# Kernel optimization log

Hardware: AMD Instinct MI355X
Metric: run time of the kernel (lower is better)

The kernel has to match this reference:

```python
import jax, jax.numpy as jnp
import numpy as np

N_NODES = 50000
NUM_HEAD = 2
NEG_SLOPE_ATT = 0.2
NEG_SLOPE_ACT = 0.3


def _glorot(key, shape):
    fan = shape[-1] + (shape[-2] if len(shape) > 1 else shape[-1])
    lim = jnp.sqrt(6.0 / fan)
    return jax.random.uniform(key, shape, jnp.float32, -lim, lim)


def gat_conv(h, src, dst, W, att, bias):
    # h: (N, in_dim); W: (out_dim, in_dim) torch Linear layout; att: (1, H, 2k)
    N = h.shape[0]
    H = att.shape[1]
    k = att.shape[2] // 2
    x = (h @ W.T).reshape(N, H, k)
    x_i = x[dst]  # target features (E, H, k)
    x_j = x[src]  # source features (E, H, k)
    # alpha = sum(cat([x_i, x_j]) * att) without materializing the concat
    alpha = jnp.einsum('ehk,hk->eh', x_i, att[0, :, :k]) + jnp.einsum('ehk,hk->eh', x_j, att[0, :, k:])
    alpha = jax.nn.leaky_relu(alpha, NEG_SLOPE_ATT)
    # segment softmax grouped by edge_index[0] (src), as in the original code
    m = jax.ops.segment_max(alpha, src, num_segments=N)
    e = jnp.exp(alpha - m[src])
    s = jax.ops.segment_sum(e, src, num_segments=N)
    alpha = e / (s[src] + 1e-16)
    msg = x_j * alpha[:, :, None]
    out = jax.ops.segment_sum(msg, dst, num_segments=N)  # aggregate to targets
    out = out.reshape(N, H * k) + bias
    return jax.nn.relu(out)


def _forward(x, src, dst, node_index, params):
    (W1, att1, b1, W2, att2, b2, W3, att3, b3, W_out, b_out) = params
    h = gat_conv(x, src, dst, W1, att1, b1)
    h = jax.nn.leaky_relu(h, NEG_SLOPE_ACT)
    h = gat_conv(h, src, dst, W2, att2, b2)
    h = jax.nn.leaky_relu(h, NEG_SLOPE_ACT)
    h = gat_conv(h, src, dst, W3, att3, b3)
    x_embed = jax.nn.leaky_relu(h, NEG_SLOPE_ACT)
    output = x_embed @ W_out.T + b_out
    node_output = output[node_index]
    ypred = jnp.argmax(output, axis=1)
    y_nodepred = ypred[node_index]
    return x_embed, node_output, ypred, y_nodepred


def setup_inputs() -> dict:
    key = jax.random.key(0)
    ks = jax.random.split(key, 16)
    N, E, D = N_NODES, 800000, 128
    H, k = NUM_HEAD, 128 // NUM_HEAD
    inp = {
        'x': jax.random.normal(ks[0], (N, D), jnp.float32),
        'edge_index': jax.random.randint(ks[1], (2, E), 0, N, jnp.int64),
        'node_label': jax.random.normal(ks[2], (1000, 1, 3), jnp.float32),
        'node_index': jax.random.randint(ks[3], (1000,), 0, N, jnp.int64),
        'W1': _glorot(ks[4], (D, D)),
        'att1': _glorot(ks[5], (1, H, 2 * k)),
        'b1': jnp.zeros((D,), jnp.float32),
        'W2': _glorot(ks[6], (D, D)),
        'att2': _glorot(ks[7], (1, H, 2 * k)),
        'b2': jnp.zeros((D,), jnp.float32),
        'W3': _glorot(ks[8], (D, D)),
        'att3': _glorot(ks[9], (1, H, 2 * k)),
        'b3': jnp.zeros((D,), jnp.float32),
        'W_out': _glorot(ks[10], (3, D)),
        'b_out': jnp.zeros((3,), jnp.float32),
    }
    return inp


def reference(x, edge_index, node_label, node_index, W1, att1, b1, W2, att2, b2, W3, att3, b3, W_out, b_out):
    N = x.shape[0]
    loop = jnp.arange(N, dtype=edge_index.dtype)
    src = jnp.concatenate([edge_index[0], loop])  # add_self_loops
    dst = jnp.concatenate([edge_index[1], loop])
    params = (W1, att1, b1, W2, att2, b2, W3, att3, b3, W_out, b_out)
    return _forward(x, src, dst, node_index, params)
```

## Files before the change

### kernel.cpp

```cpp
#include <hip/hip_runtime.h>
#include <math.h>


#define EPB 8192

__global__ __launch_bounds__(256) void gemm128(const float* __restrict__ A,
                                               const float* __restrict__ Wm,
                                               const float* __restrict__ att,
                                               float* __restrict__ C,
                                               float4* __restrict__ ni4,
                                               float2* __restrict__ ad2v, int N) {
    __shared__ float As[64][68];
    __shared__ float Wt[64][132];
    const int tx = threadIdx.x;
    const int row0 = blockIdx.x * 64;
    const int cid = tx & 31;
    const int rid = tx >> 5;
    float acc[8][4] = {};
    const float4* A4 = (const float4*)A;
    const float4* W4 = (const float4*)Wm;

    for (int kt = 0; kt < 2; ++kt) {
        for (int i = tx; i < 1024; i += 256) {
            int r = i >> 4, q = i & 15;
            int row = row0 + r;
            float4 v = (row < N) ? A4[(size_t)row * 32 + kt * 16 + q]
                                 : make_float4(0.f, 0.f, 0.f, 0.f);
            As[r][q * 4 + 0] = v.x; As[r][q * 4 + 1] = v.y;
            As[r][q * 4 + 2] = v.z; As[r][q * 4 + 3] = v.w;
        }
        for (int i = tx; i < 2048; i += 256) {
            int c = i >> 4, q = i & 15;
            float4 v = W4[(size_t)c * 32 + kt * 16 + q];
            Wt[q * 4 + 0][c] = v.x; Wt[q * 4 + 1][c] = v.y;
            Wt[q * 4 + 2][c] = v.z; Wt[q * 4 + 3][c] = v.w;
        }
        __syncthreads();
        for (int k = 0; k < 64; k += 4) {
            float4 a[8];
            #pragma unroll
            for (int i = 0; i < 8; ++i) a[i] = *(const float4*)&As[rid * 8 + i][k];
            #pragma unroll
            for (int kk = 0; kk < 4; ++kk) {
                float4 w = *(const float4*)&Wt[k + kk][cid * 4];
                #pragma unroll
                for (int i = 0; i < 8; ++i) {
                    float av = (kk == 0) ? a[i].x : (kk == 1) ? a[i].y : (kk == 2) ? a[i].z : a[i].w;
                    acc[i][0] += av * w.x; acc[i][1] += av * w.y;
                    acc[i][2] += av * w.z; acc[i][3] += av * w.w;
                }
            }
        }
        __syncthreads();
    }
    #pragma unroll
    for (int i = 0; i < 8; ++i) {
        int row = row0 + rid * 8 + i;
        if (row < N)
            ((float4*)C)[(size_t)row * 32 + cid] =
                make_float4(acc[i][0], acc[i][1], acc[i][2], acc[i][3]);
    }
    const int hh = cid >> 4;
    const int c0 = (cid & 15) * 4;
    float ad0 = att[hh * 128 + c0 + 0], ad1 = att[hh * 128 + c0 + 1];
    float ad2c = att[hh * 128 + c0 + 2], ad3 = att[hh * 128 + c0 + 3];
    float as0 = att[hh * 128 + 64 + c0 + 0], as1 = att[hh * 128 + 64 + c0 + 1];
    float as2 = att[hh * 128 + 64 + c0 + 2], as3 = att[hh * 128 + 64 + c0 + 3];
    float pd[8], ps[8];
    #pragma unroll
    for (int i = 0; i < 8; ++i) {
        pd[i] = acc[i][0] * ad0 + acc[i][1] * ad1 + acc[i][2] * ad2c + acc[i][3] * ad3;
        ps[i] = acc[i][0] * as0 + acc[i][1] * as1 + acc[i][2] * as2 + acc[i][3] * as3;
    }
    #pragma unroll
    for (int m = 1; m < 16; m <<= 1) {
        #pragma unroll
        for (int i = 0; i < 8; ++i) {
            pd[i] += __shfl_xor(pd[i], m);
            ps[i] += __shfl_xor(ps[i], m);
        }
    }
    const int ll = tx & 63;
    const int grp = ll & 32;
    #pragma unroll
    for (int i = 0; i < 8; ++i) {
        float d0 = __shfl(pd[i], grp + 0);
        float d1 = __shfl(pd[i], grp + 16);
        float s0 = __shfl(ps[i], grp + 0);
        float s1 = __shfl(ps[i], grp + 16);
        if ((ll & 31) == 0) {
            int row = row0 + rid * 8 + i;
            if (row < N) {
                ad2v[row] = make_float2(d0, d1);
                ni4[row] = make_float4(s0, s1, 0.f, 0.f);
            }
        }
    }
}

__global__ __launch_bounds__(256) void init_deg(unsigned int* __restrict__ dd,
                                                unsigned int* __restrict__ ds, int N) {
    int n = blockIdx.x * 256 + threadIdx.x;
    if (n < N) { dd[n] = 1u; ds[n] = 1u; }
}

__global__ __launch_bounds__(256) void hist_both(const int* __restrict__ ei, int E,
                                                 unsigned int* __restrict__ dd,
                                                 unsigned int* __restrict__ ds) {
    int e = blockIdx.x * 256 + threadIdx.x;
    if (e < E) {
        atomicAdd(&ds[ei[e]], 1u);
        atomicAdd(&dd[ei[E + e]], 1u);
    }
}

__global__ __launch_bounds__(256) void scan_p1(const unsigned int* __restrict__ deg,
                                               unsigned int* __restrict__ off,
                                               unsigned int* __restrict__ bsum, int N) {
    __shared__ unsigned int sh[256];
    int t = threadIdx.x;
    int base = blockIdx.x * 1024 + t * 4;
    unsigned int v0 = 0, v1 = 0, v2 = 0, v3 = 0;
    if (base + 3 < N) {
        uint4 q = *(const uint4*)&deg[base];
        v0 = q.x; v1 = q.y; v2 = q.z; v3 = q.w;
    } else {
        if (base + 0 < N) v0 = deg[base + 0];
        if (base + 1 < N) v1 = deg[base + 1];
        if (base + 2 < N) v2 = deg[base + 2];
        if (base + 3 < N) v3 = deg[base + 3];
    }
    sh[t] = v0 + v1 + v2 + v3;
    __syncthreads();
    #pragma unroll
    for (int d = 1; d < 256; d <<= 1) {
        unsigned int u = (t >= d) ? sh[t - d] : 0u;
        __syncthreads();
        sh[t] += u;
        __syncthreads();
    }
    unsigned int ex = (t == 0) ? 0u : sh[t - 1];
    if (base + 3 < N) {
        *(uint4*)&off[base] = make_uint4(ex, ex + v0, ex + v0 + v1, ex + v0 + v1 + v2);
    } else {
        if (base + 0 < N) off[base + 0] = ex;
        if (base + 1 < N) off[base + 1] = ex + v0;
        if (base + 2 < N) off[base + 2] = ex + v0 + v1;
        if (base + 3 < N) off[base + 3] = ex + v0 + v1 + v2;
    }
    if (t == 255) bsum[blockIdx.x] = sh[255];
}

__global__ __launch_bounds__(1024) void scan_p2(unsigned int* __restrict__ bsum, int NB) {
    __shared__ unsigned int sh[1024];
    int t = threadIdx.x;
    sh[t] = (t < NB) ? bsum[t] : 0u;
    __syncthreads();
    #pragma unroll
    for (int d = 1; d < 1024; d <<= 1) {
        unsigned int u = (t >= d) ? sh[t - d] : 0u;
        __syncthreads();
        sh[t] += u;
        __syncthreads();
    }
    if (t < NB) bsum[t] = (t == 0) ? 0u : sh[t - 1];
}

__global__ __launch_bounds__(256) void scan_p3(unsigned int* __restrict__ off,
                                               const unsigned int* __restrict__ bsum,
                                               int N, unsigned int total) {
    int i = blockIdx.x * 256 + threadIdx.x;
    if (i < N) off[i] += bsum[i >> 10];
    if (i == N) off[N] = total;
}

__global__ __launch_bounds__(256) void init_cur(const unsigned int* __restrict__ off_d,
                                                const unsigned int* __restrict__ off_s,
                                                unsigned int* __restrict__ cur_d,
                                                unsigned int* __restrict__ cur_s, int CB) {
    int b = blockIdx.x * 256 + threadIdx.x;
    if (b < CB) { cur_d[b] = off_d[b * 64]; cur_s[b] = off_s[b * 64]; }
}

template <bool BYDST>
__global__ __launch_bounds__(512) void coarse_scatter(const int* __restrict__ ei, int E, int Et,
                                                      unsigned int* __restrict__ cur,
                                                      unsigned int* __restrict__ tmp, int CB) {
    __shared__ unsigned int lh[800];
    const int t = threadIdx.x;
    for (int b = t; b < CB; b += 512) lh[b] = 0u;
    __syncthreads();
    const int i0 = blockIdx.x * EPB;
    for (int i = t; i < EPB; i += 512) {
        int e = i0 + i;
        if (e < Et) {
            int k = (e < E) ? ei[BYDST ? (E + e) : e] : (e - E);
            atomicAdd(&lh[k >> 6], 1u);
        }
    }
    __syncthreads();
    for (int b = t; b < CB; b += 512) {
        unsigned int c = lh[b];
        lh[b] = atomicAdd(&cur[b], c);
    }
    __syncthreads();
    for (int i = t; i < EPB; i += 512) {
        int e = i0 + i;
        if (e < Et) {
            int s, d;
            if (e < E) { s = ei[e]; d = ei[E + e]; } else { s = d = e - E; }
            int k = BYDST ? d : s;
            int v = BYDST ? s : d;
            unsigned int pos = atomicAdd(&lh[k >> 6], 1u);
            tmp[pos] = ((unsigned int)(k & 63) << 16) | (unsigned int)v;
        }
    }
}

__global__ __launch_bounds__(256) void fine_sort(const unsigned int* __restrict__ tmp,
                                                 const unsigned int* __restrict__ off,
                                                 int* __restrict__ outv, int N) {
    __shared__ unsigned int h[64];
    const int b = blockIdx.x;
    const int node0 = b * 64;
    int nn = N - node0; if (nn > 64) nn = 64;
    const int t = threadIdx.x;
    if (t < nn) h[t] = off[node0 + t];
    __syncthreads();
    unsigned int base = off[node0];
    unsigned int end = off[node0 + nn];
    for (unsigned int i = base + t; i < end; i += 256) {
        unsigned int v = tmp[i];
        unsigned int pos = atomicAdd(&h[v >> 16], 1u);
        outv[pos] = (int)(v & 0xFFFFu);
    }
}

__global__ __launch_bounds__(256) void src_sum(const int* __restrict__ dsts,
                                               const unsigned int* __restrict__ off_s,
                                               const float2* __restrict__ ad2,
                                               float* __restrict__ ni, int N) {
    int n = blockIdx.x * 256 + threadIdx.x;
    if (n >= N) return;
    float as0 = ni[(size_t)n * 4 + 0];
    float as1 = ni[(size_t)n * 4 + 1];
    unsigned int j0 = off_s[n], j1 = off_s[n + 1];
    float s0 = 0.f, s1 = 0.f;
    unsigned int j = j0;
    for (; j + 4 <= j1; j += 4) {
        int d0 = dsts[j], d1 = dsts[j + 1], d2 = dsts[j + 2], d3 = dsts[j + 3];
        float2 a0 = ad2[d0], a1 = ad2[d1], a2 = ad2[d2], a3 = ad2[d3];
        float t;
        t = as0 + a0.x; t = (t > 0.f) ? t : 0.2f * t; s0 += __expf(t);
        t = as1 + a0.y; t = (t > 0.f) ? t : 0.2f * t; s1 += __expf(t);
        t = as0 + a1.x; t = (t > 0.f) ? t : 0.2f * t; s0 += __expf(t);
        t = as1 + a1.y; t = (t > 0.f) ? t : 0.2f * t; s1 += __expf(t);
        t = as0 + a2.x; t = (t > 0.f) ? t : 0.2f * t; s0 += __expf(t);
        t = as1 + a2.y; t = (t > 0.f) ? t : 0.2f * t; s1 += __expf(t);
        t = as0 + a3.x; t = (t > 0.f) ? t : 0.2f * t; s0 += __expf(t);
        t = as1 + a3.y; t = (t > 0.f) ? t : 0.2f * t; s1 += __expf(t);
    }
    for (; j < j1; ++j) {
        float2 a = ad2[dsts[j]];
        float t;
        t = as0 + a.x; t = (t > 0.f) ? t : 0.2f * t; s0 += __expf(t);
        t = as1 + a.y; t = (t > 0.f) ? t : 0.2f * t; s1 += __expf(t);
    }
    ni[(size_t)n * 4 + 2] = 1.0f / (s0 + 1e-16f);
    ni[(size_t)n * 4 + 3] = 1.0f / (s1 + 1e-16f);
}

template <int U>
__device__ __forceinline__ void agg_edges(unsigned int j, const int* __restrict__ srcs,
                                          const float4* __restrict__ ni4,
                                          const float2* __restrict__ x2,
                                          float2 ad, int l, int hi,
                                          float& accx, float& accy) {
    int s[U]; float4 ni[U]; float2 v[U];
    #pragma unroll
    for (int u = 0; u < U; ++u) s[u] = srcs[j + u];
    #pragma unroll
    for (int u = 0; u < U; ++u) ni[u] = ni4[s[u]];
    #pragma unroll
    for (int u = 0; u < U; ++u) v[u] = x2[(size_t)s[u] * 64 + l];
    #pragma unroll
    for (int u = 0; u < U; ++u) {
        float al0 = ad.x + ni[u].x; al0 = (al0 > 0.f) ? al0 : 0.2f * al0;
        float al1 = ad.y + ni[u].y; al1 = (al1 > 0.f) ? al1 : 0.2f * al1;
        float w = hi ? __expf(al1) * ni[u].w : __expf(al0) * ni[u].z;
        accx += v[u].x * w;
        accy += v[u].y * w;
    }
}

template <bool LAST>
__global__ __launch_bounds__(256) void agg_csr(const int* __restrict__ srcs,
                                               const unsigned int* __restrict__ off,
                                               const float2* __restrict__ x2,
                                               const float4* __restrict__ ni4,
                                               const float2* __restrict__ ad2,
                                               const float* __restrict__ bias,
                                               float* __restrict__ out,
                                               const float* __restrict__ Wout,
                                               const float* __restrict__ bout,
                                               float* __restrict__ out3,
                                               float* __restrict__ ypred, int N) {
    int d = blockIdx.x * 4 + (threadIdx.x >> 6);
    int l = threadIdx.x & 63;
    if (d >= N) return;
    d = __builtin_amdgcn_readfirstlane(d);
    const int hi = l >> 5;
    float2 ad = ad2[d];
    unsigned int j0 = off[d], j1 = off[d + 1];
    float accx = 0.f, accy = 0.f;
    unsigned int j = j0;
    for (; j + 8 <= j1; j += 8) agg_edges<8>(j, srcs, ni4, x2, ad, l, hi, accx, accy);
    if (j + 4 <= j1) { agg_edges<4>(j, srcs, ni4, x2, ad, l, hi, accx, accy); j += 4; }
    if (j + 2 <= j1) { agg_edges<2>(j, srcs, ni4, x2, ad, l, hi, accx, accy); j += 2; }
    if (j < j1)      { agg_edges<1>(j, srcs, ni4, x2, ad, l, hi, accx, accy); }

    float2 bb = ((const float2*)bias)[l];
    float o0 = fmaxf(accx + bb.x, 0.f);
    float o1 = fmaxf(accy + bb.y, 0.f);
    ((float2*)out)[(size_t)d * 64 + l] = make_float2(o0, o1);
    if (LAST) {
        const float2* W2 = (const float2*)Wout;
        float2 wa = W2[l], wb = W2[64 + l], wc = W2[128 + l];
        float p0 = o0 * wa.x + o1 * wa.y;
        float p1 = o0 * wb.x + o1 * wb.y;
        float p2 = o0 * wc.x + o1 * wc.y;
        #pragma unroll
        for (int m = 32; m; m >>= 1) {
            p0 += __shfl_xor(p0, m);
            p1 += __shfl_xor(p1, m);
            p2 += __shfl_xor(p2, m);
        }
        if (l == 0) {
            p0 += bout[0]; p1 += bout[1]; p2 += bout[2];
            out3[d * 3 + 0] = p0; out3[d * 3 + 1] = p1; out3[d * 3 + 2] = p2;
            int am = 0; float best = p0;
            if (p1 > best) { best = p1; am = 1; }
            if (p2 > best) { best = p2; am = 2; }
            ypred[d] = (float)am;
        }
    }
}

__global__ __launch_bounds__(256) void gather_out(const float* __restrict__ out3,
                                                  const float* __restrict__ ypred,
                                                  const int* __restrict__ node_index,
                                                  float* __restrict__ node_out,
                                                  float* __restrict__ y_nodepred, int M) {
    int i = blockIdx.x * 256 + threadIdx.x;
    if (i >= M) return;
    int idx = node_index[i];
    node_out[i * 3 + 0] = out3[idx * 3 + 0];
    node_out[i * 3 + 1] = out3[idx * 3 + 1];
    node_out[i * 3 + 2] = out3[idx * 3 + 2];
    y_nodepred[i] = ypred[idx];
}

extern "C" void kernel_launch(void* const* d_in, const int* in_sizes, int n_in,
                              void* d_out, int out_size, void* d_ws, size_t ws_size,
                              hipStream_t stream) {
    const float* x          = (const float*)d_in[0];
    const int*   ei         = (const int*)d_in[1];
    const int*   node_index = (const int*)d_in[3];
    const float* W[3]   = {(const float*)d_in[4], (const float*)d_in[7], (const float*)d_in[10]};
    const float* att[3] = {(const float*)d_in[5], (const float*)d_in[8], (const float*)d_in[11]};
    const float* b[3]   = {(const float*)d_in[6], (const float*)d_in[9], (const float*)d_in[12]};
    const float* Wout = (const float*)d_in[13];
    const float* bout = (const float*)d_in[14];

    const int N  = in_sizes[0] / 128;
    const int E  = in_sizes[1] / 2;
    const int Et = E + N;
    const int M  = in_sizes[3];
    const int NB = (N + 1023) / 1024;
    const int CB = (N + 63) / 64;
    const int NBLK = (Et + EPB - 1) / EPB;

    float* ws     = (float*)d_ws;
    float* xlin   = ws;
    float* hb     = xlin + (size_t)N * 128;
    float* ad     = hb + (size_t)N * 128;
    float* ni     = ad + (size_t)N * 2;
    float* out3   = ni + (size_t)N * 4;
    unsigned int* off_d = (unsigned int*)(out3 + (size_t)N * 3 + 4);
    unsigned int* off_s = off_d + (size_t)N + 4;
    unsigned int* deg_d = off_s + (size_t)N + 4;
    unsigned int* deg_s = deg_d + (size_t)N;
    unsigned int* cur_d = deg_s + (size_t)N;
    unsigned int* cur_s = cur_d + 1024;
    unsigned int* bsum_d = cur_s + 1024;
    unsigned int* bsum_s = bsum_d + 1024;
    int* srcs = (int*)(bsum_s + 1024);
    int* dsts = srcs + (size_t)Et;
    unsigned int* tmp = (unsigned int*)(dsts + (size_t)Et);

    float* o_embed = (float*)d_out;
    float* o_node  = o_embed + (size_t)N * 128;
    float* o_ypred = o_node + (size_t)M * 3;
    float* o_ynode = o_ypred + (size_t)N;

    const int gemm_blocks = (N + 63) / 64;
    const int node_wave_blocks = (N + 3) / 4;
    const int n_blocks = (N + 255) / 256;

    init_deg<<<n_blocks, 256, 0, stream>>>(deg_d, deg_s, N);
    hist_both<<<(E + 255) / 256, 256, 0, stream>>>(ei, E, deg_d, deg_s);
    scan_p1<<<NB, 256, 0, stream>>>(deg_d, off_d, bsum_d, N);
    scan_p1<<<NB, 256, 0, stream>>>(deg_s, off_s, bsum_s, N);
    scan_p2<<<1, 1024, 0, stream>>>(bsum_d, NB);
    scan_p2<<<1, 1024, 0, stream>>>(bsum_s, NB);
    scan_p3<<<(N + 256) / 256, 256, 0, stream>>>(off_d, bsum_d, N, (unsigned int)Et);
    scan_p3<<<(N + 256) / 256, 256, 0, stream>>>(off_s, bsum_s, N, (unsigned int)Et);
    init_cur<<<(CB + 255) / 256, 256, 0, stream>>>(off_d, off_s, cur_d, cur_s, CB);
    coarse_scatter<true><<<NBLK, 512, 0, stream>>>(ei, E, Et, cur_d, tmp, CB);
    fine_sort<<<CB, 256, 0, stream>>>(tmp, off_d, srcs, N);
    coarse_scatter<false><<<NBLK, 512, 0, stream>>>(ei, E, Et, cur_s, tmp, CB);
    fine_sort<<<CB, 256, 0, stream>>>(tmp, off_s, dsts, N);

    for (int L = 0; L < 3; ++L) {
        const float* hin = (L == 0) ? x : hb;
        gemm128<<<gemm_blocks, 256, 0, stream>>>(hin, W[L], att[L], xlin,
                                                 (float4*)ni, (float2*)ad, N);
        src_sum<<<n_blocks, 256, 0, stream>>>(dsts, off_s, (const float2*)ad, ni, N);
        if (L < 2)
            agg_csr<false><<<node_wave_blocks, 256, 0, stream>>>(
                srcs, off_d, (const float2*)xlin, (const float4*)ni, (const float2*)ad,
                b[L], hb, nullptr, nullptr, nullptr, nullptr, N);
        else
            agg_csr<true><<<node_wave_blocks, 256, 0, stream>>>(
                srcs, off_d, (const float2*)xlin, (const float4*)ni, (const float2*)ad,
                b[L], o_embed, Wout, bout, out3, o_ypred, N);
    }
    gather_out<<<(M + 255) / 256, 256, 0, stream>>>(out3, o_ypred, node_index, o_node, o_ynode, M);
}
```

Baseline: 478.5 us.

## Precompute per-edge attention weights, merge scan kernels, and reuse workspace buffers

Adds an edge_w kernel that computes the normalized attention weight per CSR edge once per layer. The aggregation kernel then reads a float2 weight instead of gathering ni4 and recomputing exp for all 64 lanes, and its unroll is widened to 16. The preprocessing scans for the dst and src degree arrays now run as combined launches, with init_cur folded into scan_p3 and init_deg replaced by a memset plus a +1 inside the scan. EPB is halved and the workspace is re-aliased so tmp overlaps xlin and out3 overlaps ad. The cost is an extra kernel launch and an extra E-sized write and read per layer.

```diff
diff --git a/kernel.cpp b/kernel.cpp
--- a/kernel.cpp
+++ b/kernel.cpp
@@ -2,7 +2,7 @@
 #include <math.h>
 
 
-#define EPB 8192
+#define EPB 4096
 
 __global__ __launch_bounds__(256) void gemm128(const float* __restrict__ A,
                                                const float* __restrict__ Wm,
@@ -98,12 +98,6 @@
     }
 }
 
-__global__ __launch_bounds__(256) void init_deg(unsigned int* __restrict__ dd,
-                                                unsigned int* __restrict__ ds, int N) {
-    int n = blockIdx.x * 256 + threadIdx.x;
-    if (n < N) { dd[n] = 1u; ds[n] = 1u; }
-}
-
 __global__ __launch_bounds__(256) void hist_both(const int* __restrict__ ei, int E,
                                                  unsigned int* __restrict__ dd,
                                                  unsigned int* __restrict__ ds) {
@@ -114,21 +108,30 @@
     }
 }
 
-__global__ __launch_bounds__(256) void scan_p1(const unsigned int* __restrict__ deg,
-                                               unsigned int* __restrict__ off,
-                                               unsigned int* __restrict__ bsum, int N) {
+__global__ __launch_bounds__(256) void scan_p1(const unsigned int* __restrict__ deg_d,
+                                               const unsigned int* __restrict__ deg_s,
+                                               unsigned int* __restrict__ off_dv,
+                                               unsigned int* __restrict__ off_sv,
+                                               unsigned int* __restrict__ bsum_dv,
+                                               unsigned int* __restrict__ bsum_sv,
+                                               int N, int NB) {
     __shared__ unsigned int sh[256];
+    const bool isS = (int)blockIdx.x >= NB;
+    const unsigned int* deg = isS ? deg_s : deg_d;
+    unsigned int* off  = isS ? off_sv  : off_dv;
+    unsigned int* bsum = isS ? bsum_sv : bsum_dv;
+    const int blk = isS ? (blockIdx.x - NB) : blockIdx.x;
     int t = threadIdx.x;
-    int base = blockIdx.x * 1024 + t * 4;
+    int base = blk * 1024 + t * 4;
     unsigned int v0 = 0, v1 = 0, v2 = 0, v3 = 0;
     if (base + 3 < N) {
         uint4 q = *(const uint4*)&deg[base];
-        v0 = q.x; v1 = q.y; v2 = q.z; v3 = q.w;
+        v0 = q.x + 1u; v1 = q.y + 1u; v2 = q.z + 1u; v3 = q.w + 1u;
     } else {
-        if (base + 0 < N) v0 = deg[base + 0];
-        if (base + 1 < N) v1 = deg[base + 1];
-        if (base + 2 < N) v2 = deg[base + 2];
-        if (base + 3 < N) v3 = deg[base + 3];
+        if (base + 0 < N) v0 = deg[base + 0] + 1u;
+        if (base + 1 < N) v1 = deg[base + 1] + 1u;
+        if (base + 2 < N) v2 = deg[base + 2] + 1u;
+        if (base + 3 < N) v3 = deg[base + 3] + 1u;
     }
     sh[t] = v0 + v1 + v2 + v3;
     __syncthreads();
@@ -148,11 +151,13 @@
         if (base + 2 < N) off[base + 2] = ex + v0 + v1;
         if (base + 3 < N) off[base + 3] = ex + v0 + v1 + v2;
     }
-    if (t == 255) bsum[blockIdx.x] = sh[255];
-}
-
-__global__ __launch_bounds__(1024) void scan_p2(unsigned int* __restrict__ bsum, int NB) {
+    if (t == 255) bsum[blk] = sh[255];
+}
+
+__global__ __launch_bounds__(1024) void scan_p2(unsigned int* __restrict__ bsum_d,
+                                                unsigned int* __restrict__ bsum_s, int NB) {
     __shared__ unsigned int sh[1024];
+    unsigned int* bsum = blockIdx.x ? bsum_s : bsum_d;
     int t = threadIdx.x;
     sh[t] = (t < NB) ? bsum[t] : 0u;
     __syncthreads();
@@ -166,20 +171,25 @@
     if (t < NB) bsum[t] = (t == 0) ? 0u : sh[t - 1];
 }
 
-__global__ __launch_bounds__(256) void scan_p3(unsigned int* __restrict__ off,
-                                               const unsigned int* __restrict__ bsum,
-                                               int N, unsigned int total) {
-    int i = blockIdx.x * 256 + threadIdx.x;
-    if (i < N) off[i] += bsum[i >> 10];
+__global__ __launch_bounds__(256) void scan_p3(unsigned int* __restrict__ off_dv,
+                                               unsigned int* __restrict__ off_sv,
+                                               const unsigned int* __restrict__ bsum_dv,
+                                               const unsigned int* __restrict__ bsum_sv,
+                                               unsigned int* __restrict__ cur_dv,
+                                               unsigned int* __restrict__ cur_sv,
+                                               int N, unsigned int total, int half) {
+    const bool isS = (int)blockIdx.x >= half;
+    unsigned int* off = isS ? off_sv : off_dv;
+    const unsigned int* bsum = isS ? bsum_sv : bsum_dv;
+    unsigned int* cur = isS ? cur_sv : cur_dv;
+    const int blk = isS ? (blockIdx.x - half) : blockIdx.x;
+    int i = blk * 256 + threadIdx.x;
+    if (i < N) {
+        unsigned int v = off[i] + bsum[i >> 10];
+        off[i] = v;
+        if ((i & 63) == 0) cur[i >> 6] = v;
+    }
     if (i == N) off[N] = total;
-}
-
-__global__ __launch_bounds__(256) void init_cur(const unsigned int* __restrict__ off_d,
-                                                const unsigned int* __restrict__ off_s,
-                                                unsigned int* __restrict__ cur_d,
-                                                unsigned int* __restrict__ cur_s, int CB) {
-    int b = blockIdx.x * 256 + threadIdx.x;
-    if (b < CB) { cur_d[b] = off_d[b * 64]; cur_s[b] = off_s[b * 64]; }
 }
 
 template <bool BYDST>
@@ -270,26 +280,52 @@
     ni[(size_t)n * 4 + 3] = 1.0f / (s1 + 1e-16f);
 }
 
+__global__ __launch_bounds__(256) void edge_w(const int* __restrict__ srcs,
+                                              const unsigned int* __restrict__ off_d,
+                                              const float4* __restrict__ ni4,
+                                              const float2* __restrict__ ad2,
+                                              float2* __restrict__ w2, int N) {
+    __shared__ unsigned int lb[65];
+    __shared__ float2 lad[64];
+    const int node0 = blockIdx.x * 64;
+    int nn = N - node0; if (nn > 64) nn = 64;
+    const int t = threadIdx.x;
+    if (t <= nn) lb[t] = off_d[node0 + t];
+    if (t < nn) lad[t] = ad2[node0 + t];
+    __syncthreads();
+    unsigned int base = lb[0], end = lb[nn];
+    for (unsigned int i = base + t; i < end; i += 256) {
+        int lo = 0, hi = nn;
+        while (hi - lo > 1) {
+            int mid = (lo + hi) >> 1;
+            if (i >= lb[mid]) lo = mid; else hi = mid;
+        }
+        float2 ad = lad[lo];
+        int s = srcs[i];
+        float4 nv = ni4[s];
+        float a0 = ad.x + nv.x; a0 = (a0 > 0.f) ? a0 : 0.2f * a0;
+        float a1 = ad.y + nv.y; a1 = (a1 > 0.f) ? a1 : 0.2f * a1;
+        w2[i] = make_float2(__expf(a0) * nv.z, __expf(a1) * nv.w);
+    }
+}
+
 template <int U>
 __device__ __forceinline__ void agg_edges(unsigned int j, const int* __restrict__ srcs,
-                                          const float4* __restrict__ ni4,
+                                          const float2* __restrict__ w2,
                                           const float2* __restrict__ x2,
-                                          float2 ad, int l, int hi,
-                                          float& accx, float& accy) {
-    int s[U]; float4 ni[U]; float2 v[U];
+                                          int l, int hi, float& accx, float& accy) {
+    int s[U]; float2 w[U]; float2 v[U];
     #pragma unroll
     for (int u = 0; u < U; ++u) s[u] = srcs[j + u];
     #pragma unroll
-    for (int u = 0; u < U; ++u) ni[u] = ni4[s[u]];
+    for (int u = 0; u < U; ++u) w[u] = w2[j + u];
     #pragma unroll
     for (int u = 0; u < U; ++u) v[u] = x2[(size_t)s[u] * 64 + l];
     #pragma unroll
     for (int u = 0; u < U; ++u) {
-        float al0 = ad.x + ni[u].x; al0 = (al0 > 0.f) ? al0 : 0.2f * al0;
-        float al1 = ad.y + ni[u].y; al1 = (al1 > 0.f) ? al1 : 0.2f * al1;
-        float w = hi ? __expf(al1) * ni[u].w : __expf(al0) * ni[u].z;
-        accx += v[u].x * w;
-        accy += v[u].y * w;
+        float ww = hi ? w[u].y : w[u].x;
+        accx += v[u].x * ww;
+        accy += v[u].y * ww;
     }
 }
 
@@ -297,8 +333,7 @@
 __global__ __launch_bounds__(256) void agg_csr(const int* __restrict__ srcs,
                                                const unsigned int* __restrict__ off,
                                                const float2* __restrict__ x2,
-                                               const float4* __restrict__ ni4,
-                                               const float2* __restrict__ ad2,
+                                               const float2* __restrict__ w2,
                                                const float* __restrict__ bias,
                                                float* __restrict__ out,
                                                const float* __restrict__ Wout,
@@ -310,14 +345,14 @@
     if (d >= N) return;
     d = __builtin_amdgcn_readfirstlane(d);
     const int hi = l >> 5;
-    float2 ad = ad2[d];
     unsigned int j0 = off[d], j1 = off[d + 1];
     float accx = 0.f, accy = 0.f;
     unsigned int j = j0;
-    for (; j + 8 <= j1; j += 8) agg_edges<8>(j, srcs, ni4, x2, ad, l, hi, accx, accy);
-    if (j + 4 <= j1) { agg_edges<4>(j, srcs, ni4, x2, ad, l, hi, accx, accy); j += 4; }
-    if (j + 2 <= j1) { agg_edges<2>(j, srcs, ni4, x2, ad, l, hi, accx, accy); j += 2; }
-    if (j < j1)      { agg_edges<1>(j, srcs, ni4, x2, ad, l, hi, accx, accy); }
+    for (; j + 16 <= j1; j += 16) agg_edges<16>(j, srcs, w2, x2, l, hi, accx, accy);
+    if (j + 8 <= j1) { agg_edges<8>(j, srcs, w2, x2, l, hi, accx, accy); j += 8; }
+    if (j + 4 <= j1) { agg_edges<4>(j, srcs, w2, x2, l, hi, accx, accy); j += 4; }
+    if (j + 2 <= j1) { agg_edges<2>(j, srcs, w2, x2, l, hi, accx, accy); j += 2; }
+    if (j < j1)      { agg_edges<1>(j, srcs, w2, x2, l, hi, accx, accy); }
 
     float2 bb = ((const float2*)bias)[l];
     float o0 = fmaxf(accx + bb.x, 0.f);
@@ -382,11 +417,12 @@
 
     float* ws     = (float*)d_ws;
     float* xlin   = ws;
+    unsigned int* tmp = (unsigned int*)ws;
     float* hb     = xlin + (size_t)N * 128;
     float* ad     = hb + (size_t)N * 128;
     float* ni     = ad + (size_t)N * 2;
-    float* out3   = ni + (size_t)N * 4;
-    unsigned int* off_d = (unsigned int*)(out3 + (size_t)N * 3 + 4);
+    float* out3   = ad;
+    unsigned int* off_d = (unsigned int*)(ni + (size_t)N * 4);
     unsigned int* off_s = off_d + (size_t)N + 4;
     unsigned int* deg_d = off_s + (size_t)N + 4;
     unsigned int* deg_s = deg_d + (size_t)N;
@@ -396,7 +432,7 @@
     unsigned int* bsum_s = bsum_d + 1024;
     int* srcs = (int*)(bsum_s + 1024);
     int* dsts = srcs + (size_t)Et;
-    unsigned int* tmp = (unsigned int*)(dsts + (size_t)Et);
+    float2* w2 = (float2*)(dsts + (size_t)Et);
 
     float* o_embed = (float*)d_out;
     float* o_node  = o_embed + (size_t)N * 128;
@@ -406,16 +442,14 @@
     const int gemm_blocks = (N + 63) / 64;
     const int node_wave_blocks = (N + 3) / 4;
     const int n_blocks = (N + 255) / 256;
-
-    init_deg<<<n_blocks, 256, 0, stream>>>(deg_d, deg_s, N);
+    const int p3_half = (N + 256) / 256;
+
+    hipMemsetAsync(deg_d, 0, (size_t)2 * N * sizeof(unsigned int), stream);
     hist_both<<<(E + 255) / 256, 256, 0, stream>>>(ei, E, deg_d, deg_s);
-    scan_p1<<<NB, 256, 0, stream>>>(deg_d, off_d, bsum_d, N);
-    scan_p1<<<NB, 256, 0, stream>>>(deg_s, off_s, bsum_s, N);
-    scan_p2<<<1, 1024, 0, stream>>>(bsum_d, NB);
-    scan_p2<<<1, 1024, 0, stream>>>(bsum_s, NB);
-    scan_p3<<<(N + 256) / 256, 256, 0, stream>>>(off_d, bsum_d, N, (unsigned int)Et);
-    scan_p3<<<(N + 256) / 256, 256, 0, stream>>>(off_s, bsum_s, N, (unsigned int)Et);
-    init_cur<<<(CB + 255) / 256, 256, 0, stream>>>(off_d, off_s, cur_d, cur_s, CB);
+    scan_p1<<<2 * NB, 256, 0, stream>>>(deg_d, deg_s, off_d, off_s, bsum_d, bsum_s, N, NB);
+    scan_p2<<<2, 1024, 0, stream>>>(bsum_d, bsum_s, NB);
+    scan_p3<<<2 * p3_half, 256, 0, stream>>>(off_d, off_s, bsum_d, bsum_s, cur_d, cur_s,
+                                             N, (unsigned int)Et, p3_half);
     coarse_scatter<true><<<NBLK, 512, 0, stream>>>(ei, E, Et, cur_d, tmp, CB);
     fine_sort<<<CB, 256, 0, stream>>>(tmp, off_d, srcs, N);
     coarse_scatter<false><<<NBLK, 512, 0, stream>>>(ei, E, Et, cur_s, tmp, CB);
@@ -426,13 +460,15 @@
         gemm128<<<gemm_blocks, 256, 0, stream>>>(hin, W[L], att[L], xlin,
                                                  (float4*)ni, (float2*)ad, N);
         src_sum<<<n_blocks, 256, 0, stream>>>(dsts, off_s, (const float2*)ad, ni, N);
+        edge_w<<<CB, 256, 0, stream>>>(srcs, off_d, (const float4*)ni, (const float2*)ad,
+                                       w2, N);
         if (L < 2)
             agg_csr<false><<<node_wave_blocks, 256, 0, stream>>>(
-                srcs, off_d, (const float2*)xlin, (const float4*)ni, (const float2*)ad,
+                srcs, off_d, (const float2*)xlin, (const float2*)w2,
                 b[L], hb, nullptr, nullptr, nullptr, nullptr, N);
         else
             agg_csr<true><<<node_wave_blocks, 256, 0, stream>>>(
-                srcs, off_d, (const float2*)xlin, (const float4*)ni, (const float2*)ad,
+                srcs, off_d, (const float2*)xlin, (const float2*)w2,
                 b[L], o_embed, Wout, bout, out3, o_ypred, N);
     }
     gather_out<<<(M + 255) / 256, 256, 0, stream>>>(out3, o_ypred, node_index, o_node, o_ynode, M);
```

New measurement: 471.7 us. About the same (-1.4%).
